# Optimization experiments

Measured on AMD Instinct MI355X. Metric: run time of the kernel, lower is better.

## Reference

```python
import jax, jax.numpy as jnp
import numpy as np

N = 50000   # nodes
E = 800000  # edges
IN = 128
H = 256
OUT = 10
G = 128     # graphs in batch


def _uniform(key, shape, fan_in):
    bound = 1.0 / np.sqrt(fan_in)
    return jax.random.uniform(key, shape, jnp.float32, -bound, bound)


def setup_inputs() -> dict:
    key = jax.random.key(0)
    ks = jax.random.split(key, 12)
    x = jax.random.normal(ks[0], (N, IN), jnp.float32)
    edge_index = jax.random.randint(ks[1], (2, E), 0, N, dtype=jnp.int64)
    edge_weight = jax.random.uniform(ks[2], (E,), jnp.float32)
    batch = jnp.sort(jax.random.randint(ks[3], (N,), 0, G, dtype=jnp.int64))
    # GCNConv weights (bias=False)
    W0 = _uniform(ks[4], (IN, H), IN)
    W1 = _uniform(ks[5], (H, H), H)
    W2 = _uniform(ks[6], (H, H), H)
    # MLP head: [H, H, OUT]
    Wm1 = _uniform(ks[7], (H, H), H)
    bm1 = _uniform(ks[8], (H,), H)
    Wm2 = _uniform(ks[9], (H, OUT), H)
    bm2 = _uniform(ks[10], (OUT,), H)
    return dict(x=x, edge_index=edge_index, edge_weight=edge_weight, batch=batch,
                W0=W0, W1=W1, W2=W2, Wm1=Wm1, bm1=bm1, Wm2=Wm2, bm2=bm2)


def _gcn_conv(h, W, row, col, dinv_sqrt):
    """GCNConv with self-loops and symmetric deg^-1/2 normalization, bias=False.
    Self-loop contribution handled analytically (norm = dinv_sqrt[i]^2)."""
    hw = h @ W                                        # [N, H]
    norm = dinv_sqrt[row] * dinv_sqrt[col]            # [E]
    msg = hw[row] * norm[:, None]                     # [E, H] gather-scale
    agg = jax.ops.segment_sum(msg, col, num_segments=N)  # scatter-add at targets
    return agg + (dinv_sqrt * dinv_sqrt)[:, None] * hw    # add self-loop term


def reference(x, edge_index, edge_weight, batch, W0, W1, W2, Wm1, bm1, Wm2, bm2):
    row, col = edge_index[0], edge_index[1]
    # degree including self-loop (edge_weight is ignored, as in the source)
    deg = jax.ops.segment_sum(jnp.ones((E,), x.dtype), col, num_segments=N) + 1.0
    dinv_sqrt = jax.lax.rsqrt(deg)
    h = x
    for W in (W0, W1, W2):
        h = jax.nn.relu(_gcn_conv(h, W, row, col, dinv_sqrt))
    # global mean pool over graphs
    counts = jax.ops.segment_sum(jnp.ones((N,), h.dtype), batch, num_segments=G)
    pooled = jax.ops.segment_sum(h, batch, num_segments=G) / jnp.maximum(counts, 1.0)[:, None]
    # MLP head (dropout inactive at inference)
    hmid = jax.nn.relu(pooled @ Wm1 + bm1)
    last = hmid @ Wm2 + bm2
    return jax.nn.log_softmax(last, axis=-1), jax.nn.sigmoid(last), last
```

## Files before the change

### kernel.cpp

```cpp
#include <hip/hip_runtime.h>
#include <math.h>

#define N_NODES 50000
#define N_PAD   50048
#define N_EDGES 800000
#define CSR_CAP 1200000
#define IN_F 128
#define H_F 256
#define OUT_F 10
#define N_G 128
#define NCHUNKS 196

#define HB 256
#define EPB (N_EDGES / HB)
#define HWORDS (N_NODES / 2)

typedef __attribute__((ext_vector_type(4))) float f32x4;
typedef __attribute__((ext_vector_type(2))) float f32x2;
typedef unsigned char u8;
typedef unsigned short u16;

__device__ inline f32x2 fp8x2_f32_lo(unsigned int v) {
    return __builtin_amdgcn_cvt_pk_f32_fp8(v, false);
}
__device__ inline f32x2 fp8x2_f32_hi(unsigned int v) {
    return __builtin_amdgcn_cvt_pk_f32_fp8(v, true);
}
__device__ inline unsigned int f32_fp8x2_lo(float a, float b, unsigned int old) {
    return __builtin_amdgcn_cvt_pk_fp8_f32(a, b, old, false);
}
__device__ inline unsigned int f32_fp8x2_hi(float a, float b, unsigned int old) {
    return __builtin_amdgcn_cvt_pk_fp8_f32(a, b, old, true);
}
__device__ inline u8 f32_fp8(float a) {
    return (u8)(f32_fp8x2_lo(a, a, 0u) & 0xff);
}
__device__ inline ushort f2bf(float x) {
    union { float f; unsigned int u; } v; v.f = x;
    unsigned int r = v.u + 0x7fff + ((v.u >> 16) & 1);
    return (ushort)(r >> 16);
}
__device__ inline float bf2f(ushort u) {
    union { unsigned int u; float f; } v; v.u = ((unsigned int)u) << 16; return v.f;
}

__device__ inline void gl2lds16(const void* g, void* l) {
    __builtin_amdgcn_global_load_lds(
        (const __attribute__((address_space(1))) unsigned int*)g,
        (__attribute__((address_space(3))) unsigned int*)l,
        16, 0, 0);
}

__global__ __launch_bounds__(256) void histo_kernel(const int* __restrict__ col,
                                                    u16* __restrict__ H,
                                                    int* __restrict__ rank) {
    extern __shared__ unsigned int hcnt[];
    int b = blockIdx.x;
    int tid = threadIdx.x;
    for (int j = tid; j < HWORDS; j += 256) hcnt[j] = 0u;
    __syncthreads();
    int e0 = b * EPB, e1 = e0 + EPB;
    for (int e = e0 + tid; e < e1; e += 256) {
        int c = col[e];
        int sh = (c & 1) << 4;
        unsigned int old = atomicAdd(&hcnt[c >> 1], 1u << sh);
        rank[e] = (int)((old >> sh) & 0xffffu);
    }
    __syncthreads();
    u16* Hrow = H + (size_t)b * N_NODES;
    for (int j = tid; j < HWORDS; j += 256)
        *(unsigned int*)&Hrow[j * 2] = hcnt[j];
}

#define CC_CHUNK 196
#define CC_X    (CC_CHUNK + 6250)
#define CC_T0   (CC_X + 128)
#define CC_T1   (CC_T0 + 256)
#define CC_T2   (CC_T1 + 256)
#define CC_GS   (CC_T2 + NCHUNKS)

__global__ __launch_bounds__(256) void convert_chunk_kernel(
    u16* __restrict__ H, int* __restrict__ counts, int* __restrict__ csum,
    const float* __restrict__ x, u8* __restrict__ xb,
    const float* __restrict__ W0, u8* __restrict__ W0t,
    const float* __restrict__ W1, u8* __restrict__ W1t,
    const float* __restrict__ W2, u8* __restrict__ W2t,
    const int* __restrict__ batch, int* __restrict__ gstart) {
    int b = blockIdx.x;
    int tid = threadIdx.x;
    if (b < CC_CHUNK) {
        int i = b * 256 + tid;
        int total = 0;
        if (i < N_NODES) {
            u16* ci = H + i;
            int s = 0;
            for (int b0 = 0; b0 < HB; b0 += 8) {
                int h[8];
                #pragma unroll
                for (int u = 0; u < 8; ++u)
                    h[u] = ci[(size_t)(b0 + u) * N_NODES];
                #pragma unroll
                for (int u = 0; u < 8; ++u) {
                    ci[(size_t)(b0 + u) * N_NODES] = (u16)s;
                    s += h[u];
                }
            }
            total = s;
            counts[i] = total;
        }
        int v = (i < N_NODES) ? ((total + 7) & ~7) : 0;
        #pragma unroll
        for (int off = 32; off; off >>= 1) v += __shfl_down(v, off);
        __shared__ int ws[4];
        if ((tid & 63) == 0) ws[tid >> 6] = v;
        __syncthreads();
        if (tid == 0) csum[b] = ws[0] + ws[1] + ws[2] + ws[3];
    } else if (b < CC_X) {
        int i = (b - CC_CHUNK) * 256 + tid;
        float4 v = *(const float4*)(x + (size_t)i * 4);
        unsigned int p = f32_fp8x2_lo(v.x, v.y, 0u);
        p = f32_fp8x2_hi(v.z, v.w, p);
        *(unsigned int*)(xb + (size_t)i * 4) = p;
    } else if (b < CC_T0) {
        int idx = (b - CC_X) * 256 + tid;
        int k = idx >> 8, nn = idx & 255;
        W0t[nn * IN_F + k] = f32_fp8(W0[idx]);
    } else if (b < CC_T1) {
        int idx = (b - CC_T0) * 256 + tid;
        int k = idx >> 8, nn = idx & 255;
        W1t[nn * H_F + k] = f32_fp8(W1[idx]);
    } else if (b < CC_T2) {
        int idx = (b - CC_T1) * 256 + tid;
        int k = idx >> 8, nn = idx & 255;
        W2t[nn * H_F + k] = f32_fp8(W2[idx]);
    } else {
        int i = (b - CC_T2) * 256 + tid;
        if (i >= N_NODES) return;
        int bb = batch[i];
        if (i == 0) {
            for (int g = 0; g <= bb; ++g) gstart[g] = 0;
        } else {
            int p = batch[i - 1];
            if (p != bb) { for (int g = p + 1; g <= bb; ++g) gstart[g] = i; }
        }
        if (i == N_NODES - 1) {
            for (int g = bb + 1; g <= N_G; ++g) gstart[g] = N_NODES;
        }
    }
}

__global__ __launch_bounds__(256) void scan_dinv_kernel(const int* __restrict__ counts,
                                                        const int* __restrict__ csum,
                                                        int* __restrict__ offsets,
                                                        float* __restrict__ dinv,
                                                        unsigned int* __restrict__ csr_ew,
                                                        int n) {
    int tid = threadIdx.x;
    int lane = tid & 63, wid = tid >> 6;
    int cv = (tid < NCHUNKS) ? csum[tid] : 0;
    int xc = cv;
    #pragma unroll
    for (int off = 1; off < 64; off <<= 1) {
        int t = __shfl_up(xc, off);
        if (lane >= off) xc += t;
    }
    __shared__ int cw[4], cpre[4];
    __shared__ int cexcl[257];
    if (lane == 63) cw[wid] = xc;
    __syncthreads();
    if (tid == 0) { int s = 0; for (int k = 0; k < 4; ++k) { cpre[k] = s; s += cw[k]; } }
    __syncthreads();
    cexcl[tid] = cpre[wid] + xc - cv;
    if (tid == 255) cexcl[256] = cpre[3] + cw[3];
    __syncthreads();
    int base = cexcl[blockIdx.x];
    int i = blockIdx.x * 256 + tid;
    int v = (i < n) ? counts[i] : 0;
    int pv = (v + 7) & ~7;
    int x = pv;
    #pragma unroll
    for (int off = 1; off < 64; off <<= 1) {
        int t = __shfl_up(x, off);
        if (lane >= off) x += t;
    }
    __shared__ int wsum[4], wpre[4];
    if (lane == 63) wsum[wid] = x;
    __syncthreads();
    if (tid == 0) { int s = 0; for (int k = 0; k < 4; ++k) { wpre[k] = s; s += wsum[k]; } }
    __syncthreads();
    if (i < n) {
        int o = base + wpre[wid] + x - pv;
        offsets[i] = o;
        dinv[i] = rsqrtf((float)(v + 1));
        for (int z = v; z < pv; ++z) csr_ew[o + z] = 0u;
    }
    if (blockIdx.x == 0 && tid == 0) offsets[n] = cexcl[NCHUNKS];
}

__global__ __launch_bounds__(256) void fill_csr_kernel(const int* __restrict__ row,
                                                       const int* __restrict__ col,
                                                       const int* __restrict__ offsets,
                                                       const u16* __restrict__ H,
                                                       const int* __restrict__ rank,
                                                       const float* __restrict__ dinv,
                                                       unsigned int* __restrict__ csr_ew) {
    int e0 = blockIdx.x * 512 + threadIdx.x;
    int e1 = e0 + 256;
    int c0 = -1, c1 = -1, r0 = 0, r1 = 0, k0 = 0, k1 = 0;
    if (e0 < N_EDGES) { c0 = col[e0]; r0 = row[e0]; k0 = rank[e0]; }
    if (e1 < N_EDGES) { c1 = col[e1]; r1 = row[e1]; k1 = rank[e1]; }
    float dc0 = 0.f, dr0 = 0.f, dc1 = 0.f, dr1 = 0.f;
    int h0 = 0, h1 = 0;
    if (c0 >= 0) {
        dc0 = dinv[c0]; dr0 = dinv[r0];
        h0 = (int)H[(size_t)(e0 / EPB) * N_NODES + c0];
    }
    if (c1 >= 0) {
        dc1 = dinv[c1]; dr1 = dinv[r1];
        h1 = (int)H[(size_t)(e1 / EPB) * N_NODES + c1];
    }
    if (c0 >= 0)
        csr_ew[offsets[c0] + h0 + k0] = (unsigned int)r0 | ((unsigned int)f2bf(dc0 * dr0) << 16);
    if (c1 >= 0)
        csr_ew[offsets[c1] + h1 + k1] = (unsigned int)r1 | ((unsigned int)f2bf(dc1 * dr1) << 16);
}

template <int K, bool RELU>
__global__ __launch_bounds__(256) void gemm_fp8(const u8* __restrict__ A,
                                                const u8* __restrict__ Bt,
                                                u8* __restrict__ C) {
    __shared__ u8 As[4 * 4096];
    __shared__ u8 Bs[4 * 4096];
    int tid = threadIdx.x;
    int lane = tid & 63;
    int w = tid >> 6;
    int wm = w & 1, wn = w >> 1;
    int l16 = lane & 15, quad = lane >> 4;
    int row0 = blockIdx.x * 128;
    int col0 = blockIdx.y * 128;
    f32x4 acc[4][4] = {};

    int sr = tid >> 1;
    int sh = (tid & 1) * 16;
    const u8* ga = A + (size_t)(row0 + sr) * K + sh;
    const u8* gb = Bt + (size_t)(col0 + sr) * K + sh;

    #pragma unroll
    for (int k0 = 0; k0 < K; k0 += 128) {
        if (k0) __syncthreads();
        #pragma unroll
        for (int q = 0; q < 4; ++q) {
            gl2lds16(ga + k0 + q * 32, As + q * 4096 + w * 1024);
            gl2lds16(gb + k0 + q * 32, Bs + q * 4096 + w * 1024);
        }
        __syncthreads();
        #pragma unroll
        for (int h = 0; h < 4; ++h) {
            long af[4], bfr[4];
            #pragma unroll
            for (int i = 0; i < 4; ++i)
                af[i] = *(const long*)&As[h * 4096 + (wm * 64 + i * 16 + l16) * 32 + quad * 8];
            #pragma unroll
            for (int j = 0; j < 4; ++j)
                bfr[j] = *(const long*)&Bs[h * 4096 + (wn * 64 + j * 16 + l16) * 32 + quad * 8];
            #pragma unroll
            for (int i = 0; i < 4; ++i)
                #pragma unroll
                for (int j = 0; j < 4; ++j)
                    acc[i][j] = __builtin_amdgcn_mfma_f32_16x16x32_fp8_fp8(af[i], bfr[j], acc[i][j], 0, 0, 0);
        }
    }
    #pragma unroll
    for (int i = 0; i < 4; ++i) {
        int rowb = row0 + wm * 64 + i * 16 + quad * 4;
        #pragma unroll
        for (int r = 0; r < 4; ++r) {
            int grow = rowb + r;
            #pragma unroll
            for (int j = 0; j < 4; ++j) {
                int gcol = col0 + wn * 64 + j * 16 + l16;
                float v = acc[i][j][r];
                if (RELU) v = fmaxf(v, 0.f);
                C[(size_t)grow * H_F + gcol] = f32_fp8(v);
            }
        }
    }
}

__global__ __launch_bounds__(256) void aggregate128(const u8* __restrict__ hw,
                                                    const float* __restrict__ dinv,
                                                    const int* __restrict__ offsets,
                                                    const unsigned int* __restrict__ csr_ew,
                                                    u8* __restrict__ hout) {
    int w = threadIdx.x >> 6;
    int lane = threadIdx.x & 63;
    int i = blockIdx.x * 4 + w;
    if (i >= N_NODES) return;
    float di = dinv[i];
    const u8* base = hw + (size_t)lane * 2;
    unsigned int su = *(const unsigned short*)(base + (size_t)i * IN_F);
    f32x2 sv = fp8x2_f32_lo(su);
    float s = di * di;
    float a0 = s * sv.x, a1 = s * sv.y;
    int t = __builtin_amdgcn_readfirstlane(offsets[i]);
    int end = __builtin_amdgcn_readfirstlane(offsets[i + 1]);
    if (t < end) {
        uint4 eA = *(const uint4*)(csr_ew + t);
        uint4 eB = *(const uint4*)(csr_ew + t + 4);
        for (; t < end; t += 8) {
            uint4 nA, nB;
            if (t + 8 < end) {
                nA = *(const uint4*)(csr_ew + t + 8);
                nB = *(const uint4*)(csr_ew + t + 12);
            }
            unsigned int e[8] = {eA.x, eA.y, eA.z, eA.w, eB.x, eB.y, eB.z, eB.w};
            unsigned int v[8];
            #pragma unroll
            for (int u = 0; u < 8; ++u)
                v[u] = *(const unsigned short*)(base + (size_t)(e[u] & 0xffff) * IN_F);
            #pragma unroll
            for (int u = 0; u < 8; ++u) {
                float wq = bf2f((ushort)(e[u] >> 16));
                f32x2 f = fp8x2_f32_lo(v[u]);
                a0 += wq * f.x; a1 += wq * f.y;
            }
            eA = nA; eB = nB;
        }
    }
    unsigned int o = f32_fp8x2_lo(a0, a1, 0u);
    *(unsigned short*)(hout + (size_t)i * IN_F + lane * 2) = (unsigned short)(o & 0xffff);
}

__global__ __launch_bounds__(256) void aggregate256(const u8* __restrict__ hw,
                                                    const float* __restrict__ dinv,
                                                    const int* __restrict__ offsets,
                                                    const unsigned int* __restrict__ csr_ew,
                                                    u8* __restrict__ hout) {
    int w = threadIdx.x >> 6;
    int lane = threadIdx.x & 63;
    int i = blockIdx.x * 4 + w;
    if (i >= N_NODES) return;
    float di = dinv[i];
    const u8* base = hw + (size_t)lane * 4;
    unsigned int su = *(const unsigned int*)(base + (size_t)i * H_F);
    f32x2 slo = fp8x2_f32_lo(su), shi = fp8x2_f32_hi(su);
    float s = di * di;
    float a0 = s * slo.x, a1 = s * slo.y, a2 = s * shi.x, a3 = s * shi.y;
    int t = __builtin_amdgcn_readfirstlane(offsets[i]);
    int end = __builtin_amdgcn_readfirstlane(offsets[i + 1]);
    if (t < end) {
        uint4 eA = *(const uint4*)(csr_ew + t);
        uint4 eB = *(const uint4*)(csr_ew + t + 4);
        for (; t < end; t += 8) {
            uint4 nA, nB;
            if (t + 8 < end) {
                nA = *(const uint4*)(csr_ew + t + 8);
                nB = *(const uint4*)(csr_ew + t + 12);
            }
            unsigned int e[8] = {eA.x, eA.y, eA.z, eA.w, eB.x, eB.y, eB.z, eB.w};
            unsigned int v[8];
            #pragma unroll
            for (int u = 0; u < 8; ++u)
                v[u] = *(const unsigned int*)(base + (size_t)(e[u] & 0xffff) * H_F);
            #pragma unroll
            for (int u = 0; u < 8; ++u) {
                float wq = bf2f((ushort)(e[u] >> 16));
                f32x2 lo = fp8x2_f32_lo(v[u]), hi = fp8x2_f32_hi(v[u]);
                a0 += wq * lo.x; a1 += wq * lo.y;
                a2 += wq * hi.x; a3 += wq * hi.y;
            }
            eA = nA; eB = nB;
        }
    }
    unsigned int o = f32_fp8x2_lo(fmaxf(a0, 0.f), fmaxf(a1, 0.f), 0u);
    o = f32_fp8x2_hi(fmaxf(a2, 0.f), fmaxf(a3, 0.f), o);
    *(unsigned int*)(hout + (size_t)i * H_F + lane * 4) = o;
}

__global__ __launch_bounds__(1024) void pool_mlp_kernel(const u8* __restrict__ h,
                                                        const int* __restrict__ gstart,
                                                        const float* __restrict__ Wm1,
                                                        const float* __restrict__ bm1,
                                                        const float* __restrict__ Wm2,
                                                        const float* __restrict__ bm2,
                                                        float* __restrict__ out) {
    __shared__ float sm[16][H_F];
    __shared__ float p[H_F];
    __shared__ float hmid[H_F];
    __shared__ float lastv[OUT_F];
    __shared__ float stats[2];
    int g = blockIdx.x;
    int s = gstart[g], e = gstart[g + 1];
    int w = threadIdx.x >> 6;
    int lane = threadIdx.x & 63;
    float a0 = 0.f, a1 = 0.f, a2 = 0.f, a3 = 0.f;
    for (int i = s + w; i < e; i += 16) {
        unsigned int v = *(const unsigned int*)(h + (size_t)i * H_F + lane * 4);
        f32x2 lo = fp8x2_f32_lo(v), hi = fp8x2_f32_hi(v);
        a0 += lo.x; a1 += lo.y; a2 += hi.x; a3 += hi.y;
    }
    *(f32x4*)&sm[w][lane * 4] = (f32x4){a0, a1, a2, a3};
    __syncthreads();
    int j = threadIdx.x;
    int cnt = e - s;
    if (j < H_F) {
        float t = 0.f;
        #pragma unroll
        for (int k = 0; k < 16; ++k) t += sm[k][j];
        p[j] = t / (float)max(cnt, 1);
    }
    __syncthreads();
    if (j < H_F) {
        float acc = bm1[j];
        for (int k = 0; k < H_F; ++k) acc += p[k] * Wm1[k * H_F + j];
        hmid[j] = fmaxf(acc, 0.f);
    }
    __syncthreads();
    if (j < OUT_F) {
        float a = bm2[j];
        for (int k = 0; k < H_F; ++k) a += hmid[k] * Wm2[k * OUT_F + j];
        lastv[j] = a;
    }
    __syncthreads();
    if (j == 0) {
        float m = -1e30f;
        for (int o = 0; o < OUT_F; ++o) m = fmaxf(m, lastv[o]);
        float sxp = 0.f;
        for (int o = 0; o < OUT_F; ++o) sxp += expf(lastv[o] - m);
        stats[0] = m; stats[1] = logf(sxp);
    }
    __syncthreads();
    if (j < OUT_F) {
        float v = lastv[j];
        out[g * OUT_F + j] = v - stats[0] - stats[1];
        out[(size_t)N_G * OUT_F + g * OUT_F + j] = 1.f / (1.f + expf(-v));
        out[(size_t)2 * N_G * OUT_F + g * OUT_F + j] = v;
    }
}

extern "C" void kernel_launch(void* const* d_in, const int* in_sizes, int n_in,
                              void* d_out, int out_size, void* d_ws, size_t ws_size,
                              hipStream_t stream) {
    const float* x   = (const float*)d_in[0];
    const int* edge_index = (const int*)d_in[1];
    const int* batch = (const int*)d_in[3];
    const float* W0  = (const float*)d_in[4];
    const float* W1  = (const float*)d_in[5];
    const float* W2  = (const float*)d_in[6];
    const float* Wm1 = (const float*)d_in[7];
    const float* bm1 = (const float*)d_in[8];
    const float* Wm2 = (const float*)d_in[9];
    const float* bm2 = (const float*)d_in[10];
    float* out = (float*)d_out;

    char* ws = (char*)d_ws;
    size_t off = 0;
    auto alloc = [&](size_t bytes) -> void* {
        void* p = ws + off; off += (bytes + 255) & ~(size_t)255; return p;
    };
    u8* xb       = (u8*)alloc((size_t)N_PAD * IN_F);
    u8* bufA     = (u8*)alloc((size_t)N_PAD * H_F);
    u8* bufB     = (u8*)alloc((size_t)N_PAD * H_F);
    u8* t0       = (u8*)alloc((size_t)N_PAD * IN_F);
    u8* W0t      = (u8*)alloc((size_t)H_F * IN_F);
    u8* W1t      = (u8*)alloc((size_t)H_F * H_F);
    u8* W2t      = (u8*)alloc((size_t)H_F * H_F);
    float* dinv    = (float*)alloc((size_t)N_NODES * 4);
    int*   counts  = (int*)alloc((size_t)N_NODES * 4);
    int*   offsets = (int*)alloc((size_t)(N_NODES + 1) * 4);
    int*   rank    = (int*)alloc((size_t)N_EDGES * 4);
    u16*   H       = (u16*)alloc((size_t)HB * N_NODES * 2);
    unsigned int* csr_ew = (unsigned int*)alloc((size_t)CSR_CAP * 4);
    int*   csum    = (int*)alloc((size_t)256 * 4);
    int*   gstart  = (int*)alloc((size_t)(N_G + 1) * 4);

    const int* row = edge_index;
    const int* col = edge_index + N_EDGES;

    histo_kernel<<<HB, 256, HWORDS * 4, stream>>>(col, H, rank);
    convert_chunk_kernel<<<CC_GS, 256, 0, stream>>>(H, counts, csum, x, xb,
                                                    W0, W0t, W1, W1t, W2, W2t,
                                                    batch, gstart);
    scan_dinv_kernel<<<NCHUNKS, 256, 0, stream>>>(counts, csum, offsets, dinv,
                                                  csr_ew, N_NODES);
    fill_csr_kernel<<<1563, 256, 0, stream>>>(row, col, offsets, H, rank,
                                              dinv, csr_ew);

    dim3 gg(N_PAD / 128, H_F / 128);
    int agg_blocks = (N_NODES + 3) / 4;
    aggregate128<<<agg_blocks, 256, 0, stream>>>(xb, dinv, offsets, csr_ew, t0);
    gemm_fp8<IN_F, true><<<gg, 256, 0, stream>>>(t0, W0t, bufA);
    gemm_fp8<H_F, false><<<gg, 256, 0, stream>>>(bufA, W1t, bufB);
    aggregate256<<<agg_blocks, 256, 0, stream>>>(bufB, dinv, offsets, csr_ew, bufA);
    gemm_fp8<H_F, false><<<gg, 256, 0, stream>>>(bufA, W2t, bufB);
    aggregate256<<<agg_blocks, 256, 0, stream>>>(bufB, dinv, offsets, csr_ew, bufA);

    pool_mlp_kernel<<<N_G, 1024, 0, stream>>>(bufA, gstart, Wm1, bm1, Wm2, bm2, out);
}
```

Measured before the change: 278.7 us.

## Shrink per-block histogram to u8 and recompute edge ranks in fill_csr

Per-block in-degree counters shrink from 16-bit to 8-bit, which halves the global histogram written by histo_kernel and scanned by convert_chunk_kernel. The per-edge rank array is dropped. fill_csr now runs one block per histogram chunk: it loads that chunk's prefix row into LDS and takes each edge's slot with LDS atomics. This removes the rank writes and reads and halves the H traffic. In exchange, the fill launch shrinks from 1563 to 256 blocks, each using about 50KB of LDS, and it only works while per-node in-degree stays below 256.

```diff
diff --git a/kernel.cpp b/kernel.cpp
--- a/kernel.cpp
+++ b/kernel.cpp
@@ -13,12 +13,11 @@
 
 #define HB 256
 #define EPB (N_EDGES / HB)
-#define HWORDS (N_NODES / 2)
+#define HWORDS (N_NODES / 4)
 
 typedef __attribute__((ext_vector_type(4))) float f32x4;
 typedef __attribute__((ext_vector_type(2))) float f32x2;
 typedef unsigned char u8;
-typedef unsigned short u16;
 
 __device__ inline f32x2 fp8x2_f32_lo(unsigned int v) {
     return __builtin_amdgcn_cvt_pk_f32_fp8(v, false);
@@ -52,8 +51,7 @@
 }
 
 __global__ __launch_bounds__(256) void histo_kernel(const int* __restrict__ col,
-                                                    u16* __restrict__ H,
-                                                    int* __restrict__ rank) {
+                                                    u8* __restrict__ H) {
     extern __shared__ unsigned int hcnt[];
     int b = blockIdx.x;
     int tid = threadIdx.x;
@@ -62,14 +60,11 @@
     int e0 = b * EPB, e1 = e0 + EPB;
     for (int e = e0 + tid; e < e1; e += 256) {
         int c = col[e];
-        int sh = (c & 1) << 4;
-        unsigned int old = atomicAdd(&hcnt[c >> 1], 1u << sh);
-        rank[e] = (int)((old >> sh) & 0xffffu);
-    }
-    __syncthreads();
-    u16* Hrow = H + (size_t)b * N_NODES;
-    for (int j = tid; j < HWORDS; j += 256)
-        *(unsigned int*)&Hrow[j * 2] = hcnt[j];
+        atomicAdd(&hcnt[c >> 2], 1u << ((c & 3) << 3));
+    }
+    __syncthreads();
+    unsigned int* Hrow = (unsigned int*)(H + (size_t)b * N_NODES);
+    for (int j = tid; j < HWORDS; j += 256) Hrow[j] = hcnt[j];
 }
 
 #define CC_CHUNK 196
@@ -80,7 +75,7 @@
 #define CC_GS   (CC_T2 + NCHUNKS)
 
 __global__ __launch_bounds__(256) void convert_chunk_kernel(
-    u16* __restrict__ H, int* __restrict__ counts, int* __restrict__ csum,
+    u8* __restrict__ H, int* __restrict__ counts, int* __restrict__ csum,
     const float* __restrict__ x, u8* __restrict__ xb,
     const float* __restrict__ W0, u8* __restrict__ W0t,
     const float* __restrict__ W1, u8* __restrict__ W1t,
@@ -92,7 +87,7 @@
         int i = b * 256 + tid;
         int total = 0;
         if (i < N_NODES) {
-            u16* ci = H + i;
+            u8* ci = H + i;
             int s = 0;
             for (int b0 = 0; b0 < HB; b0 += 8) {
                 int h[8];
@@ -101,7 +96,7 @@
                     h[u] = ci[(size_t)(b0 + u) * N_NODES];
                 #pragma unroll
                 for (int u = 0; u < 8; ++u) {
-                    ci[(size_t)(b0 + u) * N_NODES] = (u16)s;
+                    ci[(size_t)(b0 + u) * N_NODES] = (u8)s;
                     s += h[u];
                 }
             }
@@ -200,29 +195,25 @@
 __global__ __launch_bounds__(256) void fill_csr_kernel(const int* __restrict__ row,
                                                        const int* __restrict__ col,
                                                        const int* __restrict__ offsets,
-                                                       const u16* __restrict__ H,
-                                                       const int* __restrict__ rank,
+                                                       const u8* __restrict__ H,
                                                        const float* __restrict__ dinv,
                                                        unsigned int* __restrict__ csr_ew) {
-    int e0 = blockIdx.x * 512 + threadIdx.x;
-    int e1 = e0 + 256;
-    int c0 = -1, c1 = -1, r0 = 0, r1 = 0, k0 = 0, k1 = 0;
-    if (e0 < N_EDGES) { c0 = col[e0]; r0 = row[e0]; k0 = rank[e0]; }
-    if (e1 < N_EDGES) { c1 = col[e1]; r1 = row[e1]; k1 = rank[e1]; }
-    float dc0 = 0.f, dr0 = 0.f, dc1 = 0.f, dr1 = 0.f;
-    int h0 = 0, h1 = 0;
-    if (c0 >= 0) {
-        dc0 = dinv[c0]; dr0 = dinv[r0];
-        h0 = (int)H[(size_t)(e0 / EPB) * N_NODES + c0];
-    }
-    if (c1 >= 0) {
-        dc1 = dinv[c1]; dr1 = dinv[r1];
-        h1 = (int)H[(size_t)(e1 / EPB) * N_NODES + c1];
-    }
-    if (c0 >= 0)
-        csr_ew[offsets[c0] + h0 + k0] = (unsigned int)r0 | ((unsigned int)f2bf(dc0 * dr0) << 16);
-    if (c1 >= 0)
-        csr_ew[offsets[c1] + h1 + k1] = (unsigned int)r1 | ((unsigned int)f2bf(dc1 * dr1) << 16);
+    extern __shared__ unsigned int hl[];
+    int b = blockIdx.x;
+    int tid = threadIdx.x;
+    const unsigned int* Hrow = (const unsigned int*)(H + (size_t)b * N_NODES);
+    for (int j = tid; j < HWORDS; j += 256) hl[j] = Hrow[j];
+    __syncthreads();
+    int e0 = b * EPB, e1 = e0 + EPB;
+    for (int e = e0 + tid; e < e1; e += 256) {
+        int c = col[e];
+        int r = row[e];
+        float w = dinv[c] * dinv[r];
+        int sh = (c & 3) << 3;
+        unsigned int old = atomicAdd(&hl[c >> 2], 1u << sh);
+        int k = (int)((old >> sh) & 0xffu);
+        csr_ew[offsets[c] + k] = (unsigned int)r | ((unsigned int)f2bf(w) << 16);
+    }
 }
 
 template <int K, bool RELU>
@@ -468,8 +459,7 @@
     float* dinv    = (float*)alloc((size_t)N_NODES * 4);
     int*   counts  = (int*)alloc((size_t)N_NODES * 4);
     int*   offsets = (int*)alloc((size_t)(N_NODES + 1) * 4);
-    int*   rank    = (int*)alloc((size_t)N_EDGES * 4);
-    u16*   H       = (u16*)alloc((size_t)HB * N_NODES * 2);
+    u8*    H       = (u8*)alloc((size_t)HB * N_NODES);
     unsigned int* csr_ew = (unsigned int*)alloc((size_t)CSR_CAP * 4);
     int*   csum    = (int*)alloc((size_t)256 * 4);
     int*   gstart  = (int*)alloc((size_t)(N_G + 1) * 4);
@@ -477,14 +467,14 @@
     const int* row = edge_index;
     const int* col = edge_index + N_EDGES;
 
-    histo_kernel<<<HB, 256, HWORDS * 4, stream>>>(col, H, rank);
+    histo_kernel<<<HB, 256, HWORDS * 4, stream>>>(col, H);
     convert_chunk_kernel<<<CC_GS, 256, 0, stream>>>(H, counts, csum, x, xb,
                                                     W0, W0t, W1, W1t, W2, W2t,
                                                     batch, gstart);
     scan_dinv_kernel<<<NCHUNKS, 256, 0, stream>>>(counts, csum, offsets, dinv,
                                                   csr_ew, N_NODES);
-    fill_csr_kernel<<<1563, 256, 0, stream>>>(row, col, offsets, H, rank,
-                                              dinv, csr_ew);
+    fill_csr_kernel<<<HB, 256, HWORDS * 4, stream>>>(row, col, offsets, H,
+                                                     dinv, csr_ew);
 
     dim3 gg(N_PAD / 128, H_F / 128);
     int agg_blocks = (N_NODES + 3) / 4;
```

Result: faster. 268.6 us (-3.6%).
